# Kernel tuning notes

Hardware: AMD Instinct MI355X
Metric: run time of the kernel (lower is better)

Reference implementation:

```python
import jax, jax.numpy as jnp
import numpy as np

N_NODES = 50000
N_EDGES = 800000
IN_C, HID, OUT_C, N_LAYERS = 32, 64, 8, 3

def _init(key, fan_in, shape):
    return jax.random.normal(key, shape, dtype=jnp.float32) * (1.0 / np.sqrt(fan_in))

def setup_inputs() -> dict:
    key = jax.random.key(0)
    ks = jax.random.split(key, 16)
    x = jax.random.uniform(ks[0], (N_NODES, IN_C), dtype=jnp.float32)
    edge_index = jax.random.randint(ks[1], (2, N_EDGES), 0, N_NODES, dtype=jnp.int64)
    return {
        "x": x,
        "edge_index": edge_index,
        # encoder MLP: in -> hid -> hid
        "enc_w1": _init(ks[2], IN_C, (IN_C, HID)),
        "enc_b1": jnp.zeros((HID,), jnp.float32),
        "enc_w2": _init(ks[3], HID, (HID, HID)),
        "enc_b2": jnp.zeros((HID,), jnp.float32),
        # stacked SAGEConv params: lin_l (aggregated neighbors, has bias) and lin_r (root)
        "sage_wl": _init(ks[4], HID, (N_LAYERS, HID, HID)),
        "sage_wr": _init(ks[5], HID, (N_LAYERS, HID, HID)),
        "sage_b": jnp.zeros((N_LAYERS, HID), jnp.float32),
        # decoder MLP: hid -> hid -> out
        "dec_w1": _init(ks[6], HID, (HID, HID)),
        "dec_b1": jnp.zeros((HID,), jnp.float32),
        "dec_w2": _init(ks[7], HID, (HID, OUT_C)),
        "dec_b2": jnp.zeros((OUT_C,), jnp.float32),
    }

def _gelu(x):
    return jax.nn.gelu(x, approximate=False)  # torch.nn.GELU default = exact erf

def reference(x, edge_index, enc_w1, enc_b1, enc_w2, enc_b2,
              sage_wl, sage_wr, sage_b, dec_w1, dec_b1, dec_w2, dec_b2):
    n = x.shape[0]
    src, dst = edge_index[0], edge_index[1]  # messages flow src -> dst (PyG convention)
    # in-degree counts for mean aggregation (computed once)
    deg = jax.ops.segment_sum(jnp.ones((src.shape[0],), x.dtype), dst, num_segments=n)
    inv_deg = 1.0 / jnp.maximum(deg, 1.0)

    # encoder MLP (Linear -> GELU -> Linear)
    h = _gelu(x @ enc_w1 + enc_b1) @ enc_w2 + enc_b2

    # SAGEConv + GELU blocks
    for l in range(sage_wl.shape[0]):
        agg = jax.ops.segment_sum(h[src], dst, num_segments=n) * inv_deg[:, None]
        h = _gelu(agg @ sage_wl[l] + h @ sage_wr[l] + sage_b[l])

    # decoder MLP
    out = _gelu(h @ dec_w1 + dec_b1) @ dec_w2 + dec_b2
    return out
```

## Files before the change

### kernel.cpp

```cpp
#include <hip/hip_runtime.h>
#include <math.h>

#define NN 50000
#define NE 800000
#define INC 32
#define HIDC 64
#define OUTC 8
#define NT_TILES ((NN + 63) / 64)
#define NPAD (NT_TILES * 64)
#define AS 68
#define XS 36
#define NCH 250
#define ECHK (NE / NCH)
#define BKD 128
#define NBK2 ((NN + BKD - 1) / BKD)
#define EC 12

__device__ __forceinline__ float gelu_exact(float x){
    return 0.5f * x * (1.0f + erff(x * 0.70710678118654752f));
}

template<int ST, int KK>
__device__ __forceinline__ void mm_tile(const float* __restrict__ At,
                                        const float* __restrict__ Ws,
                                        int m0, int n0, float acc[4][4])
{
    #pragma unroll 2
    for (int k = 0; k < KK; k += 2){
        float2 av[4];
        #pragma unroll
        for (int r = 0; r < 4; r++)
            av[r] = *(const float2*)&At[(m0+r)*ST + k];
        float4 w0 = *(const float4*)&Ws[(k+0)*HIDC + n0];
        float4 w1 = *(const float4*)&Ws[(k+1)*HIDC + n0];
        #pragma unroll
        for (int r = 0; r < 4; r++){
            acc[r][0] = fmaf(av[r].x, w0.x, acc[r][0]);
            acc[r][1] = fmaf(av[r].x, w0.y, acc[r][1]);
            acc[r][2] = fmaf(av[r].x, w0.z, acc[r][2]);
            acc[r][3] = fmaf(av[r].x, w0.w, acc[r][3]);
            acc[r][0] = fmaf(av[r].y, w1.x, acc[r][0]);
            acc[r][1] = fmaf(av[r].y, w1.y, acc[r][1]);
            acc[r][2] = fmaf(av[r].y, w1.z, acc[r][2]);
            acc[r][3] = fmaf(av[r].y, w1.w, acc[r][3]);
        }
    }
}


__global__ __launch_bounds__(512) void k_ebin(
    const int* __restrict__ src, const int* __restrict__ dst,
    int2* __restrict__ ebuf, int* __restrict__ cnts, int* __restrict__ lboff)
{
    __shared__ int cnt[512];
    __shared__ int cur[512];
    int c = blockIdx.x, tid = threadIdx.x;
    cnt[tid] = 0;
    __syncthreads();
    int e0 = c*ECHK;
    for (int i = e0 + tid; i < e0 + ECHK; i += 512)
        atomicAdd(&cnt[dst[i] >> 7], 1);
    __syncthreads();
    int v = cnt[tid];
    for (int off = 1; off < 512; off <<= 1){
        int t = (tid >= off) ? cnt[tid-off] : 0;
        __syncthreads();
        cnt[tid] += t;
        __syncthreads();
    }
    int excl = cnt[tid] - v;
    if (tid < NBK2){
        cnts[c*NBK2 + tid]  = v;
        lboff[c*NBK2 + tid] = excl;
    }
    cur[tid] = excl;
    __syncthreads();
    for (int i = e0 + tid; i < e0 + ECHK; i += 512){
        int d = dst[i], s = src[i];
        int p = atomicAdd(&cur[d >> 7], 1);
        ebuf[e0 + p] = make_int2(d, s);
    }
}

__global__ __launch_bounds__(256) void k_choff(
    const int* __restrict__ cnts, int* __restrict__ choff, int* __restrict__ btot)
{
    __shared__ int sd[256];
    int b = blockIdx.x, tid = threadIdx.x;
    int v = (tid < NCH) ? cnts[tid*NBK2 + b] : 0;
    sd[tid] = v;
    __syncthreads();
    for (int off = 1; off < 256; off <<= 1){
        int t = (tid >= off) ? sd[tid-off] : 0;
        __syncthreads();
        sd[tid] += t;
        __syncthreads();
    }
    if (tid < NCH) choff[b*NCH + tid] = sd[tid] - v;
    if (tid == 255) btot[b] = sd[255];
}

__global__ __launch_bounds__(512) void k_bbase(
    const int* __restrict__ btot, int* __restrict__ bbase,
    float* h0, float* h1, int* row_ptr)
{
    __shared__ int sd[512];
    int tid = threadIdx.x;
    int v = (tid < NBK2) ? btot[tid] : 0;
    sd[tid] = v;
    __syncthreads();
    for (int off = 1; off < 512; off <<= 1){
        int t = (tid >= off) ? sd[tid-off] : 0;
        __syncthreads();
        sd[tid] += t;
        __syncthreads();
    }
    if (tid < NBK2) bbase[tid] = sd[tid] - v;
    if (tid == 0) row_ptr[NN] = NE;
    if (tid < 64){
        h0[(size_t)NN*HIDC + tid] = 0.f;
        h1[(size_t)NN*HIDC + tid] = 0.f;
    }
}

__global__ __launch_bounds__(256) void k_bsort(
    const int2* __restrict__ ebuf, const int* __restrict__ lboff,
    const int* __restrict__ choff, const int* __restrict__ btot,
    const int* __restrict__ bbase,
    int* __restrict__ row_ptr, int* __restrict__ col,
    float* __restrict__ inv_deg)
{
    __shared__ int cum[NCH];
    __shared__ int lb[NCH];
    __shared__ int hcnt[BKD];
    __shared__ int fpos[BKD];
    int b = blockIdx.x, tid = threadIdx.x;
    if (tid < NCH){
        cum[tid] = choff[b*NCH + tid];
        lb[tid]  = lboff[tid*NBK2 + b];
    }
    if (tid < BKD) hcnt[tid] = 0;
    __syncthreads();
    int tot = btot[b];
    int lo = b << 7;
    int dl[EC], sv[EC];
    #pragma unroll
    for (int j = 0; j < EC; j++){
        int e = tid + j*256;
        dl[j] = -1; sv[j] = 0;
        if (e < tot){
            int lc = 0, hc = NCH;
            while (hc - lc > 1){ int mid = (lc+hc) >> 1; if (cum[mid] <= e) lc = mid; else hc = mid; }
            int2 pr = ebuf[lc*ECHK + lb[lc] + (e - cum[lc])];
            dl[j] = pr.x - lo; sv[j] = pr.y;
            atomicAdd(&hcnt[dl[j]], 1);
        }
    }
    for (int e = tid + EC*256; e < tot; e += 256){
        int lc = 0, hc = NCH;
        while (hc - lc > 1){ int mid = (lc+hc) >> 1; if (cum[mid] <= e) lc = mid; else hc = mid; }
        int2 pr = ebuf[lc*ECHK + lb[lc] + (e - cum[lc])];
        atomicAdd(&hcnt[pr.x - lo], 1);
    }
    __syncthreads();
    int v = (tid < BKD) ? hcnt[tid] : 0;
    for (int off = 1; off < BKD; off <<= 1){
        int t = (tid >= off && tid < BKD) ? hcnt[tid-off] : 0;
        __syncthreads();
        if (tid < BKD) hcnt[tid] += t;
        __syncthreads();
    }
    int base = bbase[b];
    if (tid < BKD){
        int excl = hcnt[tid] - v;
        int g = lo + tid;
        if (g < NN){
            row_ptr[g] = base + excl;
            inv_deg[g] = 1.0f / (float)max(v, 1);
        }
        fpos[tid] = base + excl;
    }
    __syncthreads();
    #pragma unroll
    for (int j = 0; j < EC; j++){
        if (dl[j] >= 0){
            int q = atomicAdd(&fpos[dl[j]], 1);
            col[q] = sv[j];
        }
    }
    for (int e = tid + EC*256; e < tot; e += 256){
        int lc = 0, hc = NCH;
        while (hc - lc > 1){ int mid = (lc+hc) >> 1; if (cum[mid] <= e) lc = mid; else hc = mid; }
        int2 pr = ebuf[lc*ECHK + lb[lc] + (e - cum[lc])];
        int q = atomicAdd(&fpos[pr.x - lo], 1);
        col[q] = pr.y;
    }
}

__global__ __launch_bounds__(256) void k_agg(
    const float* __restrict__ h_in,
    const int* __restrict__ row_ptr, const int* __restrict__ col,
    const float* __restrict__ inv_deg,
    float* __restrict__ agg)
{
    int tid = threadIdx.x;
    int wv = tid >> 6, f = tid & 63;
    int g = f >> 4, qoff = (f & 15) * 4;
    for (int node = blockIdx.x*4 + wv; node < NN; node += gridDim.x*4){
        int s0 = row_ptr[node], s1 = row_ptr[node+1];
        float a0 = 0.f, a1 = 0.f, a2 = 0.f, a3 = 0.f;
        float b0 = 0.f, b1 = 0.f, b2 = 0.f, b3 = 0.f;
        for (int p0 = s0; p0 < s1; p0 += 64){
            int cnt = s1 - p0; if (cnt > 64) cnt = 64;
            int cidx = (f < cnt) ? col[p0 + f] : NN;
            int nq = (cnt + 3) >> 2;
            int t = 0;
            for (; t + 2 <= nq; t += 2){
                int si0 = __shfl(cidx, (t+0)*4 + g);
                int si1 = __shfl(cidx, (t+1)*4 + g);
                float4 v0 = *(const float4*)&h_in[(size_t)si0*HIDC + qoff];
                float4 v1 = *(const float4*)&h_in[(size_t)si1*HIDC + qoff];
                a0 += v0.x; a1 += v0.y; a2 += v0.z; a3 += v0.w;
                b0 += v1.x; b1 += v1.y; b2 += v1.z; b3 += v1.w;
            }
            if (t < nq){
                int si0 = __shfl(cidx, t*4 + g);
                float4 v0 = *(const float4*)&h_in[(size_t)si0*HIDC + qoff];
                a0 += v0.x; a1 += v0.y; a2 += v0.z; a3 += v0.w;
            }
        }
        a0 += b0; a1 += b1; a2 += b2; a3 += b3;
        a0 += __shfl_xor(a0, 16); a0 += __shfl_xor(a0, 32);
        a1 += __shfl_xor(a1, 16); a1 += __shfl_xor(a1, 32);
        a2 += __shfl_xor(a2, 16); a2 += __shfl_xor(a2, 32);
        a3 += __shfl_xor(a3, 16); a3 += __shfl_xor(a3, 32);
        if (g == 0){
            float idg = inv_deg[node];
            float4 o = make_float4(a0*idg, a1*idg, a2*idg, a3*idg);
            *(float4*)&agg[(size_t)node*HIDC + qoff] = o;
        }
    }
}


__global__ __launch_bounds__(256) void k_enc(
    const float* __restrict__ x,
    const float* __restrict__ w1, const float* __restrict__ b1,
    const float* __restrict__ w2, const float* __restrict__ b2,
    float* __restrict__ h)
{
    __shared__ float w1s[INC*HIDC];
    __shared__ float w2s[HIDC*HIDC];
    __shared__ float Xt[64*XS];
    __shared__ float T[64*AS];
    int tid = threadIdx.x, tile = blockIdx.x;
    for (int i = tid*4; i < INC*HIDC;  i += 1024)
        *(float4*)&w1s[i] = *(const float4*)&w1[i];
    for (int i = tid*4; i < HIDC*HIDC; i += 1024)
        *(float4*)&w2s[i] = *(const float4*)&w2[i];
    for (int i = tid*4; i < 64*INC; i += 1024){
        int m = i >> 5, k = i & 31;
        int row = tile*64 + m; if (row >= NN) row = NN-1;
        *(float4*)&Xt[m*XS + k] = *(const float4*)&x[(size_t)row*INC + k];
    }
    __syncthreads();
    int tx = tid & 15, ty = tid >> 4;
    int m0 = ty*4, n0 = tx*4;
    float4 b1v = *(const float4*)&b1[n0];
    float acc[4][4];
    #pragma unroll
    for (int r = 0; r < 4; r++){
        acc[r][0]=b1v.x; acc[r][1]=b1v.y; acc[r][2]=b1v.z; acc[r][3]=b1v.w;
    }
    mm_tile<XS, INC>(Xt, w1s, m0, n0, acc);
    #pragma unroll
    for (int r = 0; r < 4; r++){
        float4 o = make_float4(gelu_exact(acc[r][0]), gelu_exact(acc[r][1]),
                               gelu_exact(acc[r][2]), gelu_exact(acc[r][3]));
        *(float4*)&T[(m0+r)*AS + n0] = o;
    }
    __syncthreads();
    float4 b2v = *(const float4*)&b2[n0];
    #pragma unroll
    for (int r = 0; r < 4; r++){
        acc[r][0]=b2v.x; acc[r][1]=b2v.y; acc[r][2]=b2v.z; acc[r][3]=b2v.w;
    }
    mm_tile<AS, HIDC>(T, w2s, m0, n0, acc);
    #pragma unroll
    for (int r = 0; r < 4; r++){
        int node = tile*64 + m0 + r;
        if (node < NN)
            *(float4*)&h[(size_t)node*HIDC + n0] =
                make_float4(acc[r][0], acc[r][1], acc[r][2], acc[r][3]);
    }
}

__global__ __launch_bounds__(256) void k_sage(
    const float* __restrict__ h_in, const float* __restrict__ agg,
    const float* __restrict__ wl, const float* __restrict__ wr,
    const float* __restrict__ bias, float* __restrict__ h_out)
{
    __shared__ float Wl[HIDC*HIDC];
    __shared__ float Wr[HIDC*HIDC];
    __shared__ float At[64*AS];
    int tid = threadIdx.x, tile = blockIdx.x;
    for (int i = tid*4; i < HIDC*HIDC; i += 1024){
        *(float4*)&Wl[i] = *(const float4*)&wl[i];
        *(float4*)&Wr[i] = *(const float4*)&wr[i];
    }
    const float* abase = agg + (size_t)tile*64*HIDC;
    for (int i = tid*4; i < 64*HIDC; i += 1024){
        int m = i >> 6, k = i & 63;
        *(float4*)&At[m*AS + k] = *(const float4*)&abase[i];
    }
    __syncthreads();
    int tx = tid & 15, ty = tid >> 4;
    int m0 = ty*4, n0 = tx*4;
    float4 bv = *(const float4*)&bias[n0];
    float acc[4][4];
    #pragma unroll
    for (int r = 0; r < 4; r++){
        acc[r][0]=bv.x; acc[r][1]=bv.y; acc[r][2]=bv.z; acc[r][3]=bv.w;
    }
    mm_tile<AS, HIDC>(At, Wl, m0, n0, acc);
    __syncthreads();
    const float* hbase = h_in + (size_t)tile*64*HIDC;
    for (int i = tid*4; i < 64*HIDC; i += 1024){
        int m = i >> 6, k = i & 63;
        *(float4*)&At[m*AS + k] = *(const float4*)&hbase[i];
    }
    __syncthreads();
    mm_tile<AS, HIDC>(At, Wr, m0, n0, acc);
    #pragma unroll
    for (int r = 0; r < 4; r++){
        int node = tile*64 + m0 + r;
        if (node < NN)
            *(float4*)&h_out[(size_t)node*HIDC + n0] =
                make_float4(gelu_exact(acc[r][0]), gelu_exact(acc[r][1]),
                            gelu_exact(acc[r][2]), gelu_exact(acc[r][3]));
    }
}

__global__ __launch_bounds__(256) void k_dec(
    const float* __restrict__ hbuf,
    const float* __restrict__ w1, const float* __restrict__ b1,
    const float* __restrict__ w2, const float* __restrict__ b2,
    float* __restrict__ out)
{
    __shared__ float w1s[HIDC*HIDC];
    __shared__ float w2s[HIDC*OUTC];
    __shared__ float At[64*AS];
    __shared__ float T[64*AS];
    int tid = threadIdx.x, tile = blockIdx.x;
    for (int i = tid*4; i < HIDC*HIDC; i += 1024)
        *(float4*)&w1s[i] = *(const float4*)&w1[i];
    if (tid*4 < HIDC*OUTC)
        *(float4*)&w2s[tid*4] = *(const float4*)&w2[tid*4];
    const float* hbase = hbuf + (size_t)tile*64*HIDC;
    for (int i = tid*4; i < 64*HIDC; i += 1024){
        int m = i >> 6, k = i & 63;
        *(float4*)&At[m*AS + k] = *(const float4*)&hbase[i];
    }
    __syncthreads();
    int tx = tid & 15, ty = tid >> 4;
    int m0 = ty*4, n0 = tx*4;
    float4 b1v = *(const float4*)&b1[n0];
    float acc[4][4];
    #pragma unroll
    for (int r = 0; r < 4; r++){
        acc[r][0]=b1v.x; acc[r][1]=b1v.y; acc[r][2]=b1v.z; acc[r][3]=b1v.w;
    }
    mm_tile<AS, HIDC>(At, w1s, m0, n0, acc);
    #pragma unroll
    for (int r = 0; r < 4; r++){
        float4 o = make_float4(gelu_exact(acc[r][0]), gelu_exact(acc[r][1]),
                               gelu_exact(acc[r][2]), gelu_exact(acc[r][3]));
        *(float4*)&T[(m0+r)*AS + n0] = o;
    }
    __syncthreads();
    int m = tid >> 2, c0 = (tid & 3) * 2;
    float a0 = b2[c0], a1 = b2[c0+1];
    #pragma unroll 4
    for (int k = 0; k < HIDC; k++){
        float tv = T[m*AS + k];
        float2 wv = *(const float2*)&w2s[k*OUTC + c0];
        a0 = fmaf(tv, wv.x, a0);
        a1 = fmaf(tv, wv.y, a1);
    }
    int node = tile*64 + m;
    if (node < NN)
        *(float2*)&out[(size_t)node*OUTC + c0] = make_float2(a0, a1);
}

extern "C" void kernel_launch(void* const* d_in, const int* in_sizes, int n_in,
                              void* d_out, int out_size, void* d_ws, size_t ws_size,
                              hipStream_t stream){
    const float* x      = (const float*)d_in[0];
    const int*   ei     = (const int*)  d_in[1];
    const float* enc_w1 = (const float*)d_in[2];
    const float* enc_b1 = (const float*)d_in[3];
    const float* enc_w2 = (const float*)d_in[4];
    const float* enc_b2 = (const float*)d_in[5];
    const float* sage_wl= (const float*)d_in[6];
    const float* sage_wr= (const float*)d_in[7];
    const float* sage_b = (const float*)d_in[8];
    const float* dec_w1 = (const float*)d_in[9];
    const float* dec_b1 = (const float*)d_in[10];
    const float* dec_w2 = (const float*)d_in[11];
    const float* dec_b2 = (const float*)d_in[12];
    float* out = (float*)d_out;

    char* ws = (char*)d_ws;
    size_t off = 0;
    auto alloc = [&](size_t bytes)->void*{
        void* p = ws + off; off = (off + bytes + 255) & ~(size_t)255; return p;
    };
    int*   cnts     = (int*)  alloc((size_t)NCH*NBK2*4);
    int*   lboff    = (int*)  alloc((size_t)NCH*NBK2*4);
    int*   choff    = (int*)  alloc((size_t)NBK2*NCH*4);
    int*   btot     = (int*)  alloc((size_t)NBK2*4);
    int*   bbase    = (int*)  alloc((size_t)NBK2*4);
    int*   row_ptr  = (int*)  alloc((size_t)(NN+1)*4);
    int*   col      = (int*)  alloc((size_t)NE*4);
    float* inv_deg  = (float*)alloc((size_t)NN*4);
    float* h0       = (float*)alloc((size_t)NPAD*HIDC*4);
    float* h1       = (float*)alloc((size_t)NPAD*HIDC*4);
    float* agg      = (float*)alloc((size_t)NPAD*HIDC*4);
    int2*  ebuf     = (int2*)agg;

    const int* srcv = ei;
    const int* dstv = ei + NE;

    hipLaunchKernelGGL(k_ebin,  dim3(NCH),  dim3(512), 0, stream,
                       srcv, dstv, ebuf, cnts, lboff);
    hipLaunchKernelGGL(k_choff, dim3(NBK2), dim3(256), 0, stream,
                       cnts, choff, btot);
    hipLaunchKernelGGL(k_bbase, dim3(1),    dim3(512), 0, stream,
                       btot, bbase, h0, h1, row_ptr);
    hipLaunchKernelGGL(k_bsort, dim3(NBK2), dim3(256), 0, stream,
                       ebuf, lboff, choff, btot, bbase, row_ptr, col, inv_deg);

    hipLaunchKernelGGL(k_enc, dim3(NT_TILES), dim3(256), 0, stream,
                       x, enc_w1, enc_b1, enc_w2, enc_b2, h0);

    const float* hin = h0; float* hout = h1;
    for (int l = 0; l < 3; l++){
        hipLaunchKernelGGL(k_agg, dim3(2048), dim3(256), 0, stream,
                           hin, row_ptr, col, inv_deg, agg);
        hipLaunchKernelGGL(k_sage, dim3(NT_TILES), dim3(256), 0, stream,
                           hin, agg,
                           sage_wl + (size_t)l*HIDC*HIDC,
                           sage_wr + (size_t)l*HIDC*HIDC,
                           sage_b  + (size_t)l*HIDC,
                           hout);
        float* t = (float*)hin; hin = hout; hout = t;
    }

    hipLaunchKernelGGL(k_dec, dim3(NT_TILES), dim3(256), 0, stream,
                       hin, dec_w1, dec_b1, dec_w2, dec_b2, out);
}
```

Baseline: 220.4 us.

## Fuse per-bucket offset scan with encoder MLP and drop the bbase kernel

The per-bucket chunk-offset scan and the encoder MLP now run as one kernel, with each work type on its own range of block indices. The single-block bucket-base scan kernel is removed; each k_bsort block instead sums the btot values of the buckets before it with a block reduction. This cuts two kernel launches and the serial single-block step from the CSR build, at the cost of redundant O(NBK2) reads of btot in every sort block. The fused kernel also carries the encoder's larger shared-memory footprint into the scan blocks.

New measurement: 215.6 us. 2.2% less time.

```diff
diff --git a/kernel.cpp b/kernel.cpp
--- a/kernel.cpp
+++ b/kernel.cpp
@@ -82,51 +82,86 @@
     }
 }
 
-__global__ __launch_bounds__(256) void k_choff(
-    const int* __restrict__ cnts, int* __restrict__ choff, int* __restrict__ btot)
-{
-    __shared__ int sd[256];
-    int b = blockIdx.x, tid = threadIdx.x;
-    int v = (tid < NCH) ? cnts[tid*NBK2 + b] : 0;
-    sd[tid] = v;
-    __syncthreads();
-    for (int off = 1; off < 256; off <<= 1){
-        int t = (tid >= off) ? sd[tid-off] : 0;
-        __syncthreads();
-        sd[tid] += t;
-        __syncthreads();
-    }
-    if (tid < NCH) choff[b*NCH + tid] = sd[tid] - v;
-    if (tid == 255) btot[b] = sd[255];
-}
-
-__global__ __launch_bounds__(512) void k_bbase(
-    const int* __restrict__ btot, int* __restrict__ bbase,
-    float* h0, float* h1, int* row_ptr)
-{
-    __shared__ int sd[512];
+__global__ __launch_bounds__(256) void k_choff_enc(
+    const int* __restrict__ cnts, int* __restrict__ choff, int* __restrict__ btot,
+    const float* __restrict__ x,
+    const float* __restrict__ w1, const float* __restrict__ b1,
+    const float* __restrict__ w2, const float* __restrict__ b2,
+    float* __restrict__ h0, float* __restrict__ h1, int* __restrict__ row_ptr)
+{
+    __shared__ float w1s[INC*HIDC];
+    __shared__ float w2s[HIDC*HIDC];
+    __shared__ float Xt[64*XS];
+    __shared__ float T[64*AS];
     int tid = threadIdx.x;
-    int v = (tid < NBK2) ? btot[tid] : 0;
-    sd[tid] = v;
-    __syncthreads();
-    for (int off = 1; off < 512; off <<= 1){
-        int t = (tid >= off) ? sd[tid-off] : 0;
-        __syncthreads();
-        sd[tid] += t;
-        __syncthreads();
-    }
-    if (tid < NBK2) bbase[tid] = sd[tid] - v;
-    if (tid == 0) row_ptr[NN] = NE;
-    if (tid < 64){
-        h0[(size_t)NN*HIDC + tid] = 0.f;
-        h1[(size_t)NN*HIDC + tid] = 0.f;
+    if (blockIdx.x < NBK2){
+        int b = blockIdx.x;
+        int* sd = (int*)w1s;
+        int v = (tid < NCH) ? cnts[tid*NBK2 + b] : 0;
+        sd[tid] = v;
+        __syncthreads();
+        for (int off = 1; off < 256; off <<= 1){
+            int t = (tid >= off) ? sd[tid-off] : 0;
+            __syncthreads();
+            sd[tid] += t;
+            __syncthreads();
+        }
+        if (tid < NCH) choff[b*NCH + tid] = sd[tid] - v;
+        if (tid == 255) btot[b] = sd[255];
+        if (b == 0){
+            if (tid < 64){
+                h0[(size_t)NN*HIDC + tid] = 0.f;
+                h1[(size_t)NN*HIDC + tid] = 0.f;
+            }
+            if (tid == 64) row_ptr[NN] = NE;
+        }
+        return;
+    }
+    int tile = blockIdx.x - NBK2;
+    for (int i = tid*4; i < INC*HIDC;  i += 1024)
+        *(float4*)&w1s[i] = *(const float4*)&w1[i];
+    for (int i = tid*4; i < HIDC*HIDC; i += 1024)
+        *(float4*)&w2s[i] = *(const float4*)&w2[i];
+    for (int i = tid*4; i < 64*INC; i += 1024){
+        int m = i >> 5, k = i & 31;
+        int row = tile*64 + m; if (row >= NN) row = NN-1;
+        *(float4*)&Xt[m*XS + k] = *(const float4*)&x[(size_t)row*INC + k];
+    }
+    __syncthreads();
+    int tx = tid & 15, ty = tid >> 4;
+    int m0 = ty*4, n0 = tx*4;
+    float4 b1v = *(const float4*)&b1[n0];
+    float acc[4][4];
+    #pragma unroll
+    for (int r = 0; r < 4; r++){
+        acc[r][0]=b1v.x; acc[r][1]=b1v.y; acc[r][2]=b1v.z; acc[r][3]=b1v.w;
+    }
+    mm_tile<XS, INC>(Xt, w1s, m0, n0, acc);
+    #pragma unroll
+    for (int r = 0; r < 4; r++){
+        float4 o = make_float4(gelu_exact(acc[r][0]), gelu_exact(acc[r][1]),
+                               gelu_exact(acc[r][2]), gelu_exact(acc[r][3]));
+        *(float4*)&T[(m0+r)*AS + n0] = o;
+    }
+    __syncthreads();
+    float4 b2v = *(const float4*)&b2[n0];
+    #pragma unroll
+    for (int r = 0; r < 4; r++){
+        acc[r][0]=b2v.x; acc[r][1]=b2v.y; acc[r][2]=b2v.z; acc[r][3]=b2v.w;
+    }
+    mm_tile<AS, HIDC>(T, w2s, m0, n0, acc);
+    #pragma unroll
+    for (int r = 0; r < 4; r++){
+        int node = tile*64 + m0 + r;
+        if (node < NN)
+            *(float4*)&h0[(size_t)node*HIDC + n0] =
+                make_float4(acc[r][0], acc[r][1], acc[r][2], acc[r][3]);
     }
 }
 
 __global__ __launch_bounds__(256) void k_bsort(
     const int2* __restrict__ ebuf, const int* __restrict__ lboff,
     const int* __restrict__ choff, const int* __restrict__ btot,
-    const int* __restrict__ bbase,
     int* __restrict__ row_ptr, int* __restrict__ col,
     float* __restrict__ inv_deg)
 {
@@ -134,13 +169,22 @@
     __shared__ int lb[NCH];
     __shared__ int hcnt[BKD];
     __shared__ int fpos[BKD];
+    __shared__ int red[256];
     int b = blockIdx.x, tid = threadIdx.x;
+    int part = 0;
+    for (int i = tid; i < b; i += 256) part += btot[i];
+    red[tid] = part;
     if (tid < NCH){
         cum[tid] = choff[b*NCH + tid];
         lb[tid]  = lboff[tid*NBK2 + b];
     }
     if (tid < BKD) hcnt[tid] = 0;
     __syncthreads();
+    for (int off = 128; off > 0; off >>= 1){
+        if (tid < off) red[tid] += red[tid + off];
+        __syncthreads();
+    }
+    int base = red[0];
     int tot = btot[b];
     int lo = b << 7;
     int dl[EC], sv[EC];
@@ -170,7 +214,6 @@
         if (tid < BKD) hcnt[tid] += t;
         __syncthreads();
     }
-    int base = bbase[b];
     if (tid < BKD){
         int excl = hcnt[tid] - v;
         int g = lo + tid;
@@ -243,58 +286,6 @@
 }
 
 
-__global__ __launch_bounds__(256) void k_enc(
-    const float* __restrict__ x,
-    const float* __restrict__ w1, const float* __restrict__ b1,
-    const float* __restrict__ w2, const float* __restrict__ b2,
-    float* __restrict__ h)
-{
-    __shared__ float w1s[INC*HIDC];
-    __shared__ float w2s[HIDC*HIDC];
-    __shared__ float Xt[64*XS];
-    __shared__ float T[64*AS];
-    int tid = threadIdx.x, tile = blockIdx.x;
-    for (int i = tid*4; i < INC*HIDC;  i += 1024)
-        *(float4*)&w1s[i] = *(const float4*)&w1[i];
-    for (int i = tid*4; i < HIDC*HIDC; i += 1024)
-        *(float4*)&w2s[i] = *(const float4*)&w2[i];
-    for (int i = tid*4; i < 64*INC; i += 1024){
-        int m = i >> 5, k = i & 31;
-        int row = tile*64 + m; if (row >= NN) row = NN-1;
-        *(float4*)&Xt[m*XS + k] = *(const float4*)&x[(size_t)row*INC + k];
-    }
-    __syncthreads();
-    int tx = tid & 15, ty = tid >> 4;
-    int m0 = ty*4, n0 = tx*4;
-    float4 b1v = *(const float4*)&b1[n0];
-    float acc[4][4];
-    #pragma unroll
-    for (int r = 0; r < 4; r++){
-        acc[r][0]=b1v.x; acc[r][1]=b1v.y; acc[r][2]=b1v.z; acc[r][3]=b1v.w;
-    }
-    mm_tile<XS, INC>(Xt, w1s, m0, n0, acc);
-    #pragma unroll
-    for (int r = 0; r < 4; r++){
-        float4 o = make_float4(gelu_exact(acc[r][0]), gelu_exact(acc[r][1]),
-                               gelu_exact(acc[r][2]), gelu_exact(acc[r][3]));
-        *(float4*)&T[(m0+r)*AS + n0] = o;
-    }
-    __syncthreads();
-    float4 b2v = *(const float4*)&b2[n0];
-    #pragma unroll
-    for (int r = 0; r < 4; r++){
-        acc[r][0]=b2v.x; acc[r][1]=b2v.y; acc[r][2]=b2v.z; acc[r][3]=b2v.w;
-    }
-    mm_tile<AS, HIDC>(T, w2s, m0, n0, acc);
-    #pragma unroll
-    for (int r = 0; r < 4; r++){
-        int node = tile*64 + m0 + r;
-        if (node < NN)
-            *(float4*)&h[(size_t)node*HIDC + n0] =
-                make_float4(acc[r][0], acc[r][1], acc[r][2], acc[r][3]);
-    }
-}
-
 __global__ __launch_bounds__(256) void k_sage(
     const float* __restrict__ h_in, const float* __restrict__ agg,
     const float* __restrict__ wl, const float* __restrict__ wr,
@@ -419,7 +410,6 @@
     int*   lboff    = (int*)  alloc((size_t)NCH*NBK2*4);
     int*   choff    = (int*)  alloc((size_t)NBK2*NCH*4);
     int*   btot     = (int*)  alloc((size_t)NBK2*4);
-    int*   bbase    = (int*)  alloc((size_t)NBK2*4);
     int*   row_ptr  = (int*)  alloc((size_t)(NN+1)*4);
     int*   col      = (int*)  alloc((size_t)NE*4);
     float* inv_deg  = (float*)alloc((size_t)NN*4);
@@ -431,17 +421,13 @@
     const int* srcv = ei;
     const int* dstv = ei + NE;
 
-    hipLaunchKernelGGL(k_ebin,  dim3(NCH),  dim3(512), 0, stream,
+    hipLaunchKernelGGL(k_ebin, dim3(NCH), dim3(512), 0, stream,
                        srcv, dstv, ebuf, cnts, lboff);
-    hipLaunchKernelGGL(k_choff, dim3(NBK2), dim3(256), 0, stream,
-                       cnts, choff, btot);
-    hipLaunchKernelGGL(k_bbase, dim3(1),    dim3(512), 0, stream,
-                       btot, bbase, h0, h1, row_ptr);
+    hipLaunchKernelGGL(k_choff_enc, dim3(NBK2 + NT_TILES), dim3(256), 0, stream,
+                       cnts, choff, btot,
+                       x, enc_w1, enc_b1, enc_w2, enc_b2, h0, h1, row_ptr);
     hipLaunchKernelGGL(k_bsort, dim3(NBK2), dim3(256), 0, stream,
-                       ebuf, lboff, choff, btot, bbase, row_ptr, col, inv_deg);
-
-    hipLaunchKernelGGL(k_enc, dim3(NT_TILES), dim3(256), 0, stream,
-                       x, enc_w1, enc_b1, enc_w2, enc_b2, h0);
+                       ebuf, lboff, choff, btot, row_ptr, col, inv_deg);
 
     const float* hin = h0; float* hout = h1;
     for (int l = 0; l < 3; l++){
```
